# Optimization experiments

Hardware: AMD Instinct MI355X
Metric: run time of the kernel (lower is better)

Reference implementation:

```python
import jax, jax.numpy as jnp
import numpy as np

N = 8192        # num neurons
D = 512         # neuron_state_size
NEG = -1e30     # finite mask value (avoids inf-inf NaNs, matches empty-predecessor -> zero output)


def setup_inputs() -> dict:
    key = jax.random.key(0)
    ks = jax.random.split(key, 5)
    neuron_states = jax.random.normal(ks[0], (N, D), dtype=jnp.float32)
    # sparse-ish directed adjacency; adjacency[i, j] True => i is a predecessor of j
    adjacency = jax.random.bernoulli(ks[1], 0.05, (N, N))
    Wq = jax.random.normal(ks[2], (D, D), dtype=jnp.float32) / np.sqrt(D)
    Wk = jax.random.normal(ks[3], (D, D), dtype=jnp.float32) / np.sqrt(D)
    Wv = jax.random.normal(ks[4], (D, D), dtype=jnp.float32) / np.sqrt(D)
    return {"neuron_states": neuron_states, "adjacency": adjacency, "Wq": Wq, "Wk": Wk, "Wv": Wv}


def reference(neuron_states, adjacency, Wq, Wk, Wv):
    # nn.Linear(bias=False): y = x @ W.T
    q = neuron_states @ Wq.T          # [N, D]
    k = neuron_states @ Wk.T          # [N, D]
    v = neuron_states @ Wv.T          # [N, D]
    # score[j, i] = q_j . k_i, valid iff adjacency[i, j] (i is predecessor of j)
    mask = adjacency.T                # [N_dst, N_src]
    scores = jnp.where(mask, q @ k.T, NEG)
    attn = jax.nn.softmax(scores, axis=1)
    attn = jnp.where(mask, attn, 0.0)  # neurons with no predecessors -> zero output (matches torch empty matmul)
    return attn @ v                   # [N, D]
```

## Files before the change

kernel.cpp:

```cpp
#include <hip/hip_runtime.h>
#include <stdint.h>

#define N 8192
#define D 512
#define NEG -1e30f

typedef _Float16 f16;
typedef f16 f16x4 __attribute__((ext_vector_type(4)));
typedef f16 f16x8 __attribute__((ext_vector_type(8)));
typedef float f32x4v __attribute__((ext_vector_type(4)));
typedef float f32x16 __attribute__((ext_vector_type(16)));

#define XH_OFF   0ull
#define WQH_OFF  (XH_OFF + 8192ull * 512 * 2)
#define WKH_OFF  (WQH_OFF + 512ull * 512 * 2)
#define WVH_OFF  (WKH_OFF + 512ull * 512 * 2)
#define QH_OFF   (WVH_OFF + 512ull * 512 * 2)
#define KH_OFF   (QH_OFF + 8192ull * 512 * 2)
#define VT_OFF   (KH_OFF + 8192ull * 512 * 2)
#define PART_SZ  (8192ull * 512 * 2)
#define P123_OFF (VT_OFF + 8192ull * 512 * 2)

#define QROW     1040
#define QS_OFF   0
#define PROW     144
#define PSB_OFF  66560
#define MLXM_OFF (PSB_OFF + 64 * PROW)
#define MLXL_OFF (MLXM_OFF + 1024)
#define MROW_OFF (MLXL_OFF + 1024)
#define LROW_OFF (MROW_OFF + 256)
#define SCL_OFF  (LROW_OFF + 256)
#define LDSB_V4  (SCL_OFF + 256)

__global__ __launch_bounds__(256) void cvt_fp16(
    const float* __restrict__ X,
    const float* __restrict__ Wq, const float* __restrict__ Wk, const float* __restrict__ Wv,
    f16* __restrict__ Xh,
    f16* __restrict__ Wqh, f16* __restrict__ Wkh, f16* __restrict__ Wvh)
{
    const int idx = blockIdx.x * 256 + threadIdx.x;
    const float* src; f16* dst; int off;
    if (idx < 1048576)      { src = X;  dst = Xh;  off = idx; }
    else if (idx < 1114112) { src = Wq; dst = Wqh; off = idx - 1048576; }
    else if (idx < 1179648) { src = Wk; dst = Wkh; off = idx - 1114112; }
    else                    { src = Wv; dst = Wvh; off = idx - 1179648; }
    const float4 v = ((const float4*)src)[off];
    f16x4 h; h.x = (f16)v.x; h.y = (f16)v.y; h.z = (f16)v.z; h.w = (f16)v.w;
    *(f16x4*)(dst + (size_t)off * 4) = h;
}

__global__ __launch_bounds__(256) void qkv_mfma(
    const f16* __restrict__ Xh,
    const f16* __restrict__ Wqh, const f16* __restrict__ Wkh, const f16* __restrict__ Wvh,
    f16* __restrict__ qh, f16* __restrict__ kh, f16* __restrict__ vt)
{
    const int t    = threadIdx.x;
    const int w    = t >> 6;
    const int lane = t & 63;
    const int lo   = lane & 31;
    const int hi   = lane >> 5;
    const int z    = blockIdx.z;

    int m0, c0; const f16 *Ap, *Bp; f16* Yp; size_t ldy;
    if (z == 2) {
        m0 = blockIdx.x * 128 + w * 32; c0 = blockIdx.y * 128;
        Ap = Wvh; Bp = Xh; Yp = vt; ldy = N;
    } else {
        m0 = blockIdx.y * 128 + w * 32; c0 = blockIdx.x * 128;
        Ap = Xh; Bp = z ? Wkh : Wqh; Yp = z ? kh : qh; ldy = D;
    }

    const f16* arow = Ap + (size_t)(m0 + lo) * D + hi * 8;
    const f16* brow[4];
#pragma unroll
    for (int nn = 0; nn < 4; ++nn)
        brow[nn] = Bp + (size_t)(c0 + nn * 32 + lo) * D + hi * 8;

    f32x16 acc[4];
#pragma unroll
    for (int nn = 0; nn < 4; ++nn)
#pragma unroll
        for (int e = 0; e < 16; ++e) acc[nn][e] = 0.f;

#pragma unroll 4
    for (int ks = 0; ks < 32; ++ks) {
        const f16x8 a = *(const f16x8*)(arow + ks * 16);
#pragma unroll
        for (int nn = 0; nn < 4; ++nn) {
            const f16x8 b = *(const f16x8*)(brow[nn] + ks * 16);
            acc[nn] = __builtin_amdgcn_mfma_f32_32x32x16_f16(a, b, acc[nn], 0, 0, 0);
        }
    }

#pragma unroll
    for (int nn = 0; nn < 4; ++nn)
#pragma unroll
        for (int r = 0; r < 16; ++r) {
            const int row = m0 + (r & 3) + 8 * (r >> 2) + 4 * hi;
            Yp[(size_t)row * ldy + c0 + nn * 32 + lo] = (f16)acc[nn][r];
        }
}

__global__ __launch_bounds__(256, 2) void attn_v4(
    const f16* __restrict__ qh, const f16* __restrict__ kh,
    const f16* __restrict__ vt, const int* __restrict__ adj,
    f16* __restrict__ part0, f16* __restrict__ part123, float2* __restrict__ ml)
{
    extern __shared__ char smem[];
    char*  Qs   = smem + QS_OFF;
    char*  Psb  = smem + PSB_OFF;
    float* mlxm = (float*)(smem + MLXM_OFF);
    float* mlxl = (float*)(smem + MLXL_OFF);
    float* mrow = (float*)(smem + MROW_OFF);
    float* lrow = (float*)(smem + LROW_OFF);
    float* scl  = (float*)(smem + SCL_OFF);

    const int t  = threadIdx.x;
    const int w  = t >> 6;
    const int l  = t & 63;
    const int cl = l & 15;
    const int hq = l >> 4;

    const int nib = gridDim.x >> 7;
    const int b   = blockIdx.x;
    const int xcd = b & 7;
    int ib, jt_;
    if (nib == 4) { ib = xcd >> 1; jt_ = (xcd & 1) * 64 + (b >> 3); }
    else          { ib = xcd >> 2; jt_ = (xcd & 3) * 32 + (b >> 3); }
    const int j0    = jt_ * 64;
    const int ibase = ib * (N / nib);
    const int iters = (N / nib) >> 6;

    f16* pb = (ib == 0) ? part0 : part123 + (size_t)(ib - 1) * ((size_t)N * D);

    for (int c = t; c < 64 * 64; c += 256) {
        const int row = c >> 6, off = c & 63;
        f16x8 v = *(const f16x8*)(qh + (size_t)(j0 + row) * D + off * 8);
        *(f16x8*)(Qs + row * QROW + off * 16) = v;
    }
    if (t < 64) { mrow[t] = NEG; lrow[t] = 0.f; }
    __syncthreads();

    f32x4v oacc[4][8];
#pragma unroll
    for (int jt = 0; jt < 4; ++jt)
#pragma unroll
        for (int dt = 0; dt < 8; ++dt) {
            oacc[jt][dt][0] = 0.f; oacc[jt][dt][1] = 0.f;
            oacc[jt][dt][2] = 0.f; oacc[jt][dt][3] = 0.f;
        }

    const char* qbase[4];
#pragma unroll
    for (int jt = 0; jt < 4; ++jt) qbase[jt] = Qs + (jt * 16 + cl) * QROW;
    const int qoff = hq * 16;

    for (int it = 0; it < iters; ++it) {
        const int i0t = ibase + it * 64;

        f32x4v sacc[4];
#pragma unroll
        for (int jt = 0; jt < 4; ++jt) {
            sacc[jt][0] = 0.f; sacc[jt][1] = 0.f; sacc[jt][2] = 0.f; sacc[jt][3] = 0.f;
        }
        const f16* kp = kh + (size_t)(i0t + w * 16 + cl) * D + hq * 8;
#pragma unroll 4
        for (int ks = 0; ks < 16; ++ks) {
            const f16x8 kf = *(const f16x8*)(kp + ks * 32);
#pragma unroll
            for (int jt = 0; jt < 4; ++jt) {
                const f16x8 qf = *(const f16x8*)(qbase[jt] + ks * 64 + qoff);
                sacc[jt] = __builtin_amdgcn_mfma_f32_16x16x32_f16(kf, qf, sacc[jt], 0, 0, 0);
            }
        }

        const int* ap = adj + (size_t)(i0t + w * 16 + hq * 4) * N + j0 + cl;
        float pe[4][4], mb[4];
#pragma unroll
        for (int jt = 0; jt < 4; ++jt) {
            int mk[4];
#pragma unroll
            for (int r = 0; r < 4; ++r) mk[r] = ap[(size_t)r * N + jt * 16];
            float s[4];
#pragma unroll
            for (int r = 0; r < 4; ++r) s[r] = mk[r] ? sacc[jt][r] : NEG;
            float m4 = fmaxf(fmaxf(s[0], s[1]), fmaxf(s[2], s[3]));
            m4 = fmaxf(m4, __shfl_xor(m4, 16, 64));
            m4 = fmaxf(m4, __shfl_xor(m4, 32, 64));
            mb[jt] = m4;
            float pl = 0.f;
#pragma unroll
            for (int r = 0; r < 4; ++r) {
                const float p = mk[r] ? __expf(s[r] - m4) : 0.f;
                pe[jt][r] = p;
                pl += p;
            }
            pl += __shfl_xor(pl, 16, 64);
            pl += __shfl_xor(pl, 32, 64);
            if (l < 16) {
                mlxm[w * 64 + jt * 16 + l] = m4;
                mlxl[w * 64 + jt * 16 + l] = pl;
            }
        }
        __syncthreads();

        if (t < 64) {
            const float mo = mrow[t];
            const float m0b = mlxm[t],       l0b = mlxl[t];
            const float m1b = mlxm[64 + t],  l1b = mlxl[64 + t];
            const float m2b = mlxm[128 + t], l2b = mlxl[128 + t];
            const float m3b = mlxm[192 + t], l3b = mlxl[192 + t];
            const float mn = fmaxf(mo, fmaxf(fmaxf(m0b, m1b), fmaxf(m2b, m3b)));
            const float ln = lrow[t] * __expf(mo - mn)
                           + l0b * __expf(m0b - mn) + l1b * __expf(m1b - mn)
                           + l2b * __expf(m2b - mn) + l3b * __expf(m3b - mn);
            mrow[t] = mn; lrow[t] = ln; scl[t] = __expf(mo - mn);
        }
        __syncthreads();

#pragma unroll
        for (int jt = 0; jt < 4; ++jt) {
            const f32x4v sc4 = *(const f32x4v*)(scl + jt * 16 + hq * 4);
#pragma unroll
            for (int dt = 0; dt < 8; ++dt) {
                oacc[jt][dt][0] *= sc4[0]; oacc[jt][dt][1] *= sc4[1];
                oacc[jt][dt][2] *= sc4[2]; oacc[jt][dt][3] *= sc4[3];
            }
            const float mn = mrow[jt * 16 + cl];
            const float f  = __expf(mb[jt] - mn);
            union { f16 h[4]; uint2 u; } pc;
#pragma unroll
            for (int r = 0; r < 4; ++r) pc.h[r] = (f16)(pe[jt][r] * f);
            *(uint2*)(Psb + (jt * 16 + cl) * PROW + (w * 16 + hq * 4) * 2) = pc.u;
        }
        __syncthreads();

        f16x8 pa[4][2];
#pragma unroll
        for (int jt = 0; jt < 4; ++jt)
#pragma unroll
            for (int k2 = 0; k2 < 2; ++k2)
                pa[jt][k2] = *(const f16x8*)(Psb + (jt * 16 + cl) * PROW + k2 * 64 + hq * 16);

#pragma unroll
        for (int dt = 0; dt < 8; ++dt) {
            const f16* vp = vt + (size_t)(w * 128 + dt * 16 + cl) * N + i0t + hq * 8;
#pragma unroll
            for (int k2 = 0; k2 < 2; ++k2) {
                const f16x8 vf = *(const f16x8*)(vp + k2 * 32);
#pragma unroll
                for (int jt = 0; jt < 4; ++jt)
                    oacc[jt][dt] = __builtin_amdgcn_mfma_f32_16x16x32_f16(pa[jt][k2], vf, oacc[jt][dt], 0, 0, 0);
            }
        }
        __syncthreads();
    }

#pragma unroll
    for (int jt = 0; jt < 4; ++jt)
#pragma unroll
        for (int dt = 0; dt < 8; ++dt)
#pragma unroll
            for (int r = 0; r < 4; ++r)
                pb[(size_t)(j0 + jt * 16 + hq * 4 + r) * D + w * 128 + dt * 16 + cl] =
                    (f16)oacc[jt][dt][r];
    if (t < 64) {
        float2 v; v.x = mrow[t]; v.y = lrow[t];
        ml[(size_t)ib * N + j0 + t] = v;
    }
}

__global__ __launch_bounds__(256) void merge_p(
    float* __restrict__ out, const f16* __restrict__ p0,
    const f16* __restrict__ p123, const float2* __restrict__ ml, int nib)
{
    const int idx = blockIdx.x * 256 + threadIdx.x;
    const int j = idx >> 7;
    const int col = (idx & 127) * 4;

    float m_g = NEG;
    for (int ib = 0; ib < nib; ++ib) m_g = fmaxf(m_g, ml[(size_t)ib * N + j].x);
    float L = 0.f;
    float4 acc; acc.x = 0.f; acc.y = 0.f; acc.z = 0.f; acc.w = 0.f;
    for (int ib = 0; ib < nib; ++ib) {
        const float2 a = ml[(size_t)ib * N + j];
        const float e = __expf(a.x - m_g);
        L += e * a.y;
        const f16* pp = (ib == 0) ? p0 : p123 + (size_t)(ib - 1) * ((size_t)N * D);
        const f16x4 h = *(const f16x4*)(pp + (size_t)j * D + col);
        acc.x += e * (float)h.x; acc.y += e * (float)h.y;
        acc.z += e * (float)h.z; acc.w += e * (float)h.w;
    }
    const float inv = (L > 0.f) ? 1.f / L : 0.f;
    float4 r; r.x = acc.x * inv; r.y = acc.y * inv; r.z = acc.z * inv; r.w = acc.w * inv;
    ((float4*)out)[idx] = r;
}

extern "C" void kernel_launch(void* const* d_in, const int* in_sizes, int n_in,
                              void* d_out, int out_size, void* d_ws, size_t ws_size,
                              hipStream_t stream) {
    const float* ns  = (const float*)d_in[0];
    const int*   adj = (const int*)d_in[1];
    const float* Wq  = (const float*)d_in[2];
    const float* Wk  = (const float*)d_in[3];
    const float* Wv  = (const float*)d_in[4];

    char* ws = (char*)d_ws;
    f16*   Xh   = (f16*)(ws + XH_OFF);
    f16*   Wqh  = (f16*)(ws + WQH_OFF);
    f16*   Wkh  = (f16*)(ws + WKH_OFF);
    f16*   Wvh  = (f16*)(ws + WVH_OFF);
    f16*   qh   = (f16*)(ws + QH_OFF);
    f16*   kh   = (f16*)(ws + KH_OFF);
    f16*   vt   = (f16*)(ws + VT_OFF);
    f16*   p0   = (f16*)(ws + XH_OFF);
    f16*   p123 = (f16*)(ws + P123_OFF);
    float* out  = (float*)d_out;

    const size_t need4 = P123_OFF + 3 * PART_SZ + 4ull * N * sizeof(float2);
    int nib; size_t ml_off;
    if (ws_size >= need4) { nib = 4; ml_off = P123_OFF + 3 * PART_SZ; }
    else                  { nib = 2; ml_off = P123_OFF + 1 * PART_SZ; }
    float2* mlb = (float2*)(ws + ml_off);

    (void)hipFuncSetAttribute((const void*)attn_v4,
                              hipFuncAttributeMaxDynamicSharedMemorySize, LDSB_V4);

    cvt_fp16<<<4864, 256, 0, stream>>>(ns, Wq, Wk, Wv, Xh, Wqh, Wkh, Wvh);
    qkv_mfma<<<dim3(4, 64, 3), 256, 0, stream>>>(Xh, Wqh, Wkh, Wvh, qh, kh, vt);
    attn_v4<<<128 * nib, 256, LDSB_V4, stream>>>(qh, kh, vt, adj, p0, p123, mlb);
    merge_p<<<4096, 256, 0, stream>>>(out, p0, p123, mlb, nib);
}
```

Measured before the change: 443.7 us.

## Pack adjacency into bitmasks and retile attention to 32 queries x 128 keys

Adds a pre-pass that packs the int32 adjacency matrix into 64-bit ballot masks, so the attention kernel reads one bit per edge instead of a 4-byte int. The attention kernel is retiled to 32 destination rows per block with 128-key steps. Running max and sum now live in registers and are shared via shuffles, which removes one barrier per iteration and the dynamic LDS. Occupancy is raised to 3 blocks per CU. The trade-off is an extra kernel pass over the 256MB adjacency, plus more blocks that each re-read K and V for fewer queries.

```diff
diff --git a/kernel.cpp b/kernel.cpp
--- a/kernel.cpp
+++ b/kernel.cpp
@@ -10,6 +10,7 @@
 typedef f16 f16x8 __attribute__((ext_vector_type(8)));
 typedef float f32x4v __attribute__((ext_vector_type(4)));
 typedef float f32x16 __attribute__((ext_vector_type(16)));
+typedef unsigned long long u64;
 
 #define XH_OFF   0ull
 #define WQH_OFF  (XH_OFF + 8192ull * 512 * 2)
@@ -20,17 +21,11 @@
 #define VT_OFF   (KH_OFF + 8192ull * 512 * 2)
 #define PART_SZ  (8192ull * 512 * 2)
 #define P123_OFF (VT_OFF + 8192ull * 512 * 2)
-
-#define QROW     1040
-#define QS_OFF   0
-#define PROW     144
-#define PSB_OFF  66560
-#define MLXM_OFF (PSB_OFF + 64 * PROW)
-#define MLXL_OFF (MLXM_OFF + 1024)
-#define MROW_OFF (MLXL_OFF + 1024)
-#define LROW_OFF (MROW_OFF + 256)
-#define SCL_OFF  (LROW_OFF + 256)
-#define LDSB_V4  (SCL_OFF + 256)
+#define ML_SZ    (4ull * N * 8)
+#define ADJ_SZ   (128ull * N * 8)
+
+#define QROW 1040
+#define PROW 272
 
 __global__ __launch_bounds__(256) void cvt_fp16(
     const float* __restrict__ X,
@@ -101,19 +96,31 @@
         }
 }
 
-__global__ __launch_bounds__(256, 2) void attn_v4(
+__global__ __launch_bounds__(256) void pack_adj(
+    const int* __restrict__ adj, u64* __restrict__ adjb)
+{
+    const int widx = blockIdx.x;
+    const int wv   = threadIdx.x >> 6;
+    const int lane = threadIdx.x & 63;
+    const int jb   = blockIdx.y * 4096 + wv * 1024;
+    const int* src = adj + (size_t)(widx * 64 + lane) * N;
+    u64* dst = adjb + (size_t)widx * N;
+    for (int jj = 0; jj < 1024; ++jj) {
+        const int j = jb + jj;
+        const u64 m = __ballot(src[j] != 0);
+        if (lane == 0) dst[j] = m;
+    }
+}
+
+__global__ __launch_bounds__(256, 3) void attn_v5(
     const f16* __restrict__ qh, const f16* __restrict__ kh,
-    const f16* __restrict__ vt, const int* __restrict__ adj,
+    const f16* __restrict__ vt, const u64* __restrict__ adjb,
     f16* __restrict__ part0, f16* __restrict__ part123, float2* __restrict__ ml)
 {
-    extern __shared__ char smem[];
-    char*  Qs   = smem + QS_OFF;
-    char*  Psb  = smem + PSB_OFF;
-    float* mlxm = (float*)(smem + MLXM_OFF);
-    float* mlxl = (float*)(smem + MLXL_OFF);
-    float* mrow = (float*)(smem + MROW_OFF);
-    float* lrow = (float*)(smem + LROW_OFF);
-    float* scl  = (float*)(smem + SCL_OFF);
+    __shared__ char  Qs[32 * QROW];
+    __shared__ char  Psb[32 * PROW];
+    __shared__ float mstat[4 * 32];
+    __shared__ float lstat[4 * 32];
 
     const int t  = threadIdx.x;
     const int w  = t >> 6;
@@ -121,135 +128,160 @@
     const int cl = l & 15;
     const int hq = l >> 4;
 
-    const int nib = gridDim.x >> 7;
+    const int nib = gridDim.x >> 8;
     const int b   = blockIdx.x;
     const int xcd = b & 7;
+    const int u   = b >> 3;
     int ib, jt_;
-    if (nib == 4) { ib = xcd >> 1; jt_ = (xcd & 1) * 64 + (b >> 3); }
-    else          { ib = xcd >> 2; jt_ = (xcd & 3) * 32 + (b >> 3); }
-    const int j0    = jt_ * 64;
+    if (nib == 4) { ib = xcd >> 1; jt_ = (xcd & 1) * 128 + u; }
+    else          { ib = xcd >> 2; jt_ = (xcd & 3) * 64 + u; }
+    const int j0    = jt_ * 32;
     const int ibase = ib * (N / nib);
-    const int iters = (N / nib) >> 6;
+    const int iters = (N / nib) >> 7;
 
     f16* pb = (ib == 0) ? part0 : part123 + (size_t)(ib - 1) * ((size_t)N * D);
 
-    for (int c = t; c < 64 * 64; c += 256) {
+    for (int c = t; c < 32 * 64; c += 256) {
         const int row = c >> 6, off = c & 63;
         f16x8 v = *(const f16x8*)(qh + (size_t)(j0 + row) * D + off * 8);
         *(f16x8*)(Qs + row * QROW + off * 16) = v;
     }
-    if (t < 64) { mrow[t] = NEG; lrow[t] = 0.f; }
     __syncthreads();
 
-    f32x4v oacc[4][8];
-#pragma unroll
-    for (int jt = 0; jt < 4; ++jt)
+    float m_run = NEG, l_run = 0.f;
+
+    f32x4v oacc[2][8];
+#pragma unroll
+    for (int jt = 0; jt < 2; ++jt)
 #pragma unroll
         for (int dt = 0; dt < 8; ++dt) {
             oacc[jt][dt][0] = 0.f; oacc[jt][dt][1] = 0.f;
             oacc[jt][dt][2] = 0.f; oacc[jt][dt][3] = 0.f;
         }
 
-    const char* qbase[4];
-#pragma unroll
-    for (int jt = 0; jt < 4; ++jt) qbase[jt] = Qs + (jt * 16 + cl) * QROW;
-    const int qoff = hq * 16;
-
     for (int it = 0; it < iters; ++it) {
-        const int i0t = ibase + it * 64;
-
-        f32x4v sacc[4];
-#pragma unroll
-        for (int jt = 0; jt < 4; ++jt) {
-            sacc[jt][0] = 0.f; sacc[jt][1] = 0.f; sacc[jt][2] = 0.f; sacc[jt][3] = 0.f;
-        }
-        const f16* kp = kh + (size_t)(i0t + w * 16 + cl) * D + hq * 8;
+        const int i0t   = ibase + it * 128;
+        const int iband = i0t + w * 32;
+
+        const u64* ab = adjb + (size_t)(iband >> 6) * N + j0;
+        const u64 wd0 = ab[cl];
+        const u64 wd1 = ab[16 + cl];
+        const int hsh = (w & 1) * 32;
+
+        f32x4v sacc[2][2];
+#pragma unroll
+        for (int a = 0; a < 2; ++a)
+#pragma unroll
+            for (int c2 = 0; c2 < 2; ++c2) {
+                sacc[a][c2][0] = 0.f; sacc[a][c2][1] = 0.f;
+                sacc[a][c2][2] = 0.f; sacc[a][c2][3] = 0.f;
+            }
+        const f16* kp = kh + (size_t)(iband + cl) * D + hq * 8;
 #pragma unroll 4
         for (int ks = 0; ks < 16; ++ks) {
-            const f16x8 kf = *(const f16x8*)(kp + ks * 32);
-#pragma unroll
-            for (int jt = 0; jt < 4; ++jt) {
-                const f16x8 qf = *(const f16x8*)(qbase[jt] + ks * 64 + qoff);
-                sacc[jt] = __builtin_amdgcn_mfma_f32_16x16x32_f16(kf, qf, sacc[jt], 0, 0, 0);
+            const f16x8 kf0 = *(const f16x8*)(kp + ks * 32);
+            const f16x8 kf1 = *(const f16x8*)(kp + (size_t)16 * D + ks * 32);
+            const f16x8 qf0 = *(const f16x8*)(Qs + cl * QROW + ks * 64 + hq * 16);
+            const f16x8 qf1 = *(const f16x8*)(Qs + (16 + cl) * QROW + ks * 64 + hq * 16);
+            sacc[0][0] = __builtin_amdgcn_mfma_f32_16x16x32_f16(kf0, qf0, sacc[0][0], 0, 0, 0);
+            sacc[0][1] = __builtin_amdgcn_mfma_f32_16x16x32_f16(kf0, qf1, sacc[0][1], 0, 0, 0);
+            sacc[1][0] = __builtin_amdgcn_mfma_f32_16x16x32_f16(kf1, qf0, sacc[1][0], 0, 0, 0);
+            sacc[1][1] = __builtin_amdgcn_mfma_f32_16x16x32_f16(kf1, qf1, sacc[1][1], 0, 0, 0);
+        }
+
+        float p[2][2][4];
+        float m4[2], pl[2];
+#pragma unroll
+        for (int jt = 0; jt < 2; ++jt) {
+            const u64 wd = jt ? wd1 : wd0;
+            const uint32_t half_ = (uint32_t)(wd >> hsh);
+            float s[2][4];
+#pragma unroll
+            for (int it2 = 0; it2 < 2; ++it2) {
+                const uint32_t sub = half_ >> (it2 * 16 + hq * 4);
+#pragma unroll
+                for (int r = 0; r < 4; ++r)
+                    s[it2][r] = ((sub >> r) & 1) ? sacc[it2][jt][r] : NEG;
             }
-        }
-
-        const int* ap = adj + (size_t)(i0t + w * 16 + hq * 4) * N + j0 + cl;
-        float pe[4][4], mb[4];
-#pragma unroll
-        for (int jt = 0; jt < 4; ++jt) {
-            int mk[4];
-#pragma unroll
-            for (int r = 0; r < 4; ++r) mk[r] = ap[(size_t)r * N + jt * 16];
-            float s[4];
-#pragma unroll
-            for (int r = 0; r < 4; ++r) s[r] = mk[r] ? sacc[jt][r] : NEG;
-            float m4 = fmaxf(fmaxf(s[0], s[1]), fmaxf(s[2], s[3]));
-            m4 = fmaxf(m4, __shfl_xor(m4, 16, 64));
-            m4 = fmaxf(m4, __shfl_xor(m4, 32, 64));
-            mb[jt] = m4;
-            float pl = 0.f;
-#pragma unroll
-            for (int r = 0; r < 4; ++r) {
-                const float p = mk[r] ? __expf(s[r] - m4) : 0.f;
-                pe[jt][r] = p;
-                pl += p;
+            float m = NEG;
+#pragma unroll
+            for (int it2 = 0; it2 < 2; ++it2)
+#pragma unroll
+                for (int r = 0; r < 4; ++r) m = fmaxf(m, s[it2][r]);
+            m = fmaxf(m, __shfl_xor(m, 16, 64));
+            m = fmaxf(m, __shfl_xor(m, 32, 64));
+            m4[jt] = m;
+            float ps = 0.f;
+#pragma unroll
+            for (int it2 = 0; it2 < 2; ++it2)
+#pragma unroll
+                for (int r = 0; r < 4; ++r) {
+                    const float pe = (s[it2][r] > -1e29f) ? __expf(s[it2][r] - m) : 0.f;
+                    p[it2][jt][r] = pe;
+                    ps += pe;
+                }
+            ps += __shfl_xor(ps, 16, 64);
+            ps += __shfl_xor(ps, 32, 64);
+            pl[jt] = ps;
+        }
+        if (l < 16) {
+            mstat[w * 32 + l]      = m4[0]; lstat[w * 32 + l]      = pl[0];
+            mstat[w * 32 + 16 + l] = m4[1]; lstat[w * 32 + 16 + l] = pl[1];
+        }
+        __syncthreads();
+
+        {
+            const int jj = l & 31;
+            const float b0 = mstat[jj],       s0 = lstat[jj];
+            const float b1 = mstat[32 + jj],  s1 = lstat[32 + jj];
+            const float b2 = mstat[64 + jj],  s2 = lstat[64 + jj];
+            const float b3 = mstat[96 + jj],  s3 = lstat[96 + jj];
+            const float mn = fmaxf(m_run, fmaxf(fmaxf(b0, b1), fmaxf(b2, b3)));
+            const float sc = __expf(m_run - mn);
+            l_run = l_run * sc + s0 * __expf(b0 - mn) + s1 * __expf(b1 - mn)
+                                + s2 * __expf(b2 - mn) + s3 * __expf(b3 - mn);
+            m_run = mn;
+
+#pragma unroll
+            for (int jt = 0; jt < 2; ++jt) {
+                const float mnj = __shfl(mn, jt * 16 + cl, 64);
+                const float f   = __expf(m4[jt] - mnj);
+#pragma unroll
+                for (int it2 = 0; it2 < 2; ++it2) {
+                    union { f16 h[4]; uint2 u2; } pc;
+#pragma unroll
+                    for (int r = 0; r < 4; ++r) pc.h[r] = (f16)(p[it2][jt][r] * f);
+                    *(uint2*)(Psb + (jt * 16 + cl) * PROW +
+                              (w * 32 + it2 * 16 + hq * 4) * 2) = pc.u2;
+                }
             }
-            pl += __shfl_xor(pl, 16, 64);
-            pl += __shfl_xor(pl, 32, 64);
-            if (l < 16) {
-                mlxm[w * 64 + jt * 16 + l] = m4;
-                mlxl[w * 64 + jt * 16 + l] = pl;
-            }
+
+#pragma unroll
+            for (int jt = 0; jt < 2; ++jt)
+#pragma unroll
+                for (int r = 0; r < 4; ++r) {
+                    const float scr = __shfl(sc, jt * 16 + hq * 4 + r, 64);
+#pragma unroll
+                    for (int dt = 0; dt < 8; ++dt) oacc[jt][dt][r] *= scr;
+                }
         }
         __syncthreads();
 
-        if (t < 64) {
-            const float mo = mrow[t];
-            const float m0b = mlxm[t],       l0b = mlxl[t];
-            const float m1b = mlxm[64 + t],  l1b = mlxl[64 + t];
-            const float m2b = mlxm[128 + t], l2b = mlxl[128 + t];
-            const float m3b = mlxm[192 + t], l3b = mlxl[192 + t];
-            const float mn = fmaxf(mo, fmaxf(fmaxf(m0b, m1b), fmaxf(m2b, m3b)));
-            const float ln = lrow[t] * __expf(mo - mn)
-                           + l0b * __expf(m0b - mn) + l1b * __expf(m1b - mn)
-                           + l2b * __expf(m2b - mn) + l3b * __expf(m3b - mn);
-            mrow[t] = mn; lrow[t] = ln; scl[t] = __expf(mo - mn);
-        }
-        __syncthreads();
-
-#pragma unroll
-        for (int jt = 0; jt < 4; ++jt) {
-            const f32x4v sc4 = *(const f32x4v*)(scl + jt * 16 + hq * 4);
-#pragma unroll
-            for (int dt = 0; dt < 8; ++dt) {
-                oacc[jt][dt][0] *= sc4[0]; oacc[jt][dt][1] *= sc4[1];
-                oacc[jt][dt][2] *= sc4[2]; oacc[jt][dt][3] *= sc4[3];
-            }
-            const float mn = mrow[jt * 16 + cl];
-            const float f  = __expf(mb[jt] - mn);
-            union { f16 h[4]; uint2 u; } pc;
-#pragma unroll
-            for (int r = 0; r < 4; ++r) pc.h[r] = (f16)(pe[jt][r] * f);
-            *(uint2*)(Psb + (jt * 16 + cl) * PROW + (w * 16 + hq * 4) * 2) = pc.u;
-        }
-        __syncthreads();
-
-        f16x8 pa[4][2];
-#pragma unroll
-        for (int jt = 0; jt < 4; ++jt)
-#pragma unroll
-            for (int k2 = 0; k2 < 2; ++k2)
+        f16x8 pa[2][4];
+#pragma unroll
+        for (int jt = 0; jt < 2; ++jt)
+#pragma unroll
+            for (int k2 = 0; k2 < 4; ++k2)
                 pa[jt][k2] = *(const f16x8*)(Psb + (jt * 16 + cl) * PROW + k2 * 64 + hq * 16);
 
 #pragma unroll
         for (int dt = 0; dt < 8; ++dt) {
             const f16* vp = vt + (size_t)(w * 128 + dt * 16 + cl) * N + i0t + hq * 8;
 #pragma unroll
-            for (int k2 = 0; k2 < 2; ++k2) {
+            for (int k2 = 0; k2 < 4; ++k2) {
                 const f16x8 vf = *(const f16x8*)(vp + k2 * 32);
 #pragma unroll
-                for (int jt = 0; jt < 4; ++jt)
+                for (int jt = 0; jt < 2; ++jt)
                     oacc[jt][dt] = __builtin_amdgcn_mfma_f32_16x16x32_f16(pa[jt][k2], vf, oacc[jt][dt], 0, 0, 0);
             }
         }
@@ -257,16 +289,16 @@
     }
 
 #pragma unroll
-    for (int jt = 0; jt < 4; ++jt)
+    for (int jt = 0; jt < 2; ++jt)
 #pragma unroll
         for (int dt = 0; dt < 8; ++dt)
 #pragma unroll
             for (int r = 0; r < 4; ++r)
                 pb[(size_t)(j0 + jt * 16 + hq * 4 + r) * D + w * 128 + dt * 16 + cl] =
                     (f16)oacc[jt][dt][r];
-    if (t < 64) {
-        float2 v; v.x = mrow[t]; v.y = lrow[t];
-        ml[(size_t)ib * N + j0 + t] = v;
+    if (w == 0 && l < 32) {
+        float2 v; v.x = m_run; v.y = l_run;
+        ml[(size_t)ib * N + j0 + l] = v;
     }
 }
 
@@ -317,17 +349,16 @@
     f16*   p123 = (f16*)(ws + P123_OFF);
     float* out  = (float*)d_out;
 
-    const size_t need4 = P123_OFF + 3 * PART_SZ + 4ull * N * sizeof(float2);
+    const size_t need4 = P123_OFF + 3 * PART_SZ + ML_SZ + ADJ_SZ;
     int nib; size_t ml_off;
     if (ws_size >= need4) { nib = 4; ml_off = P123_OFF + 3 * PART_SZ; }
     else                  { nib = 2; ml_off = P123_OFF + 1 * PART_SZ; }
-    float2* mlb = (float2*)(ws + ml_off);
-
-    (void)hipFuncSetAttribute((const void*)attn_v4,
-                              hipFuncAttributeMaxDynamicSharedMemorySize, LDSB_V4);
+    float2* mlb  = (float2*)(ws + ml_off);
+    u64*    adjb = (u64*)(ws + ml_off + ML_SZ);
 
     cvt_fp16<<<4864, 256, 0, stream>>>(ns, Wq, Wk, Wv, Xh, Wqh, Wkh, Wvh);
     qkv_mfma<<<dim3(4, 64, 3), 256, 0, stream>>>(Xh, Wqh, Wkh, Wvh, qh, kh, vt);
-    attn_v4<<<128 * nib, 256, LDSB_V4, stream>>>(qh, kh, vt, adj, p0, p123, mlb);
+    pack_adj<<<dim3(128, 2), 256, 0, stream>>>(adj, adjb);
+    attn_v5<<<256 * nib, 256, 0, stream>>>(qh, kh, vt, adjb, p0, p123, mlb);
     merge_p<<<4096, 256, 0, stream>>>(out, p0, p123, mlb, nib);
 }
```

Measured after the change: 892.5 us. 2.01x slower.

## Pack adjacency into bitmasks and prefetch next tile's K and mask

Applied to the files above, without the earlier changes.

Adds a pack_adj kernel that compresses the int32 adjacency matrix into 64-bit ballot masks, so the attention kernel reads one u64 per column per 64-row tile instead of scattered int32 loads. The attention kernel also keeps the running max and sum in registers in every wave, which removes one barrier, skips the output rescale when no scale changed, and prefetches the next tile's mask and half of K during the PV phase. The cost is an extra kernel pass over the 256MB adjacency and more register pressure from the prefetch buffers.

```diff
diff --git a/kernel.cpp b/kernel.cpp
--- a/kernel.cpp
+++ b/kernel.cpp
@@ -10,6 +10,7 @@
 typedef f16 f16x8 __attribute__((ext_vector_type(8)));
 typedef float f32x4v __attribute__((ext_vector_type(4)));
 typedef float f32x16 __attribute__((ext_vector_type(16)));
+typedef unsigned long long u64;
 
 #define XH_OFF   0ull
 #define WQH_OFF  (XH_OFF + 8192ull * 512 * 2)
@@ -20,17 +21,15 @@
 #define VT_OFF   (KH_OFF + 8192ull * 512 * 2)
 #define PART_SZ  (8192ull * 512 * 2)
 #define P123_OFF (VT_OFF + 8192ull * 512 * 2)
+#define ML_SZ    (4ull * N * 8)
+#define ADJ_SZ   (128ull * N * 8)
 
 #define QROW     1040
-#define QS_OFF   0
 #define PROW     144
 #define PSB_OFF  66560
-#define MLXM_OFF (PSB_OFF + 64 * PROW)
-#define MLXL_OFF (MLXM_OFF + 1024)
-#define MROW_OFF (MLXL_OFF + 1024)
-#define LROW_OFF (MROW_OFF + 256)
-#define SCL_OFF  (LROW_OFF + 256)
-#define LDSB_V4  (SCL_OFF + 256)
+#define MST_OFF  75776
+#define LST_OFF  76800
+#define LDSB_V6  77824
 
 __global__ __launch_bounds__(256) void cvt_fp16(
     const float* __restrict__ X,
@@ -101,19 +100,32 @@
         }
 }
 
-__global__ __launch_bounds__(256, 2) void attn_v4(
+__global__ __launch_bounds__(256) void pack_adj(
+    const int* __restrict__ adj, u64* __restrict__ adjb)
+{
+    const int widx = blockIdx.x;
+    const int wv   = threadIdx.x >> 6;
+    const int lane = threadIdx.x & 63;
+    const int jb   = blockIdx.y * 4096 + wv * 1024;
+    const int* src = adj + (size_t)(widx * 64 + lane) * N;
+    u64* dst = adjb + (size_t)widx * N;
+    for (int jj = 0; jj < 1024; ++jj) {
+        const int j = jb + jj;
+        const u64 m = __ballot(src[j] != 0);
+        if (lane == 0) dst[j] = m;
+    }
+}
+
+__global__ __launch_bounds__(256, 2) void attn_v6(
     const f16* __restrict__ qh, const f16* __restrict__ kh,
-    const f16* __restrict__ vt, const int* __restrict__ adj,
+    const f16* __restrict__ vt, const u64* __restrict__ adjb,
     f16* __restrict__ part0, f16* __restrict__ part123, float2* __restrict__ ml)
 {
     extern __shared__ char smem[];
-    char*  Qs   = smem + QS_OFF;
-    char*  Psb  = smem + PSB_OFF;
-    float* mlxm = (float*)(smem + MLXM_OFF);
-    float* mlxl = (float*)(smem + MLXL_OFF);
-    float* mrow = (float*)(smem + MROW_OFF);
-    float* lrow = (float*)(smem + LROW_OFF);
-    float* scl  = (float*)(smem + SCL_OFF);
+    char*  Qs    = smem;
+    char*  Psb   = smem + PSB_OFF;
+    float* mstat = (float*)(smem + MST_OFF);
+    float* lstat = (float*)(smem + LST_OFF);
 
     const int t  = threadIdx.x;
     const int w  = t >> 6;
@@ -138,8 +150,9 @@
         f16x8 v = *(const f16x8*)(qh + (size_t)(j0 + row) * D + off * 8);
         *(f16x8*)(Qs + row * QROW + off * 16) = v;
     }
-    if (t < 64) { mrow[t] = NEG; lrow[t] = 0.f; }
     __syncthreads();
+
+    float m_run = NEG, l_run = 0.f;
 
     f32x4v oacc[4][8];
 #pragma unroll
@@ -150,10 +163,16 @@
             oacc[jt][dt][2] = 0.f; oacc[jt][dt][3] = 0.f;
         }
 
-    const char* qbase[4];
-#pragma unroll
-    for (int jt = 0; jt < 4; ++jt) qbase[jt] = Qs + (jt * 16 + cl) * QROW;
-    const int qoff = hq * 16;
+    u64   wd[4];
+    f16x8 kpre[8];
+    {
+        const u64* ab = adjb + ((size_t)(ibase >> 6)) * N + j0;
+#pragma unroll
+        for (int jt = 0; jt < 4; ++jt) wd[jt] = ab[jt * 16 + cl];
+        const f16* kp = kh + (size_t)(ibase + w * 16 + cl) * D + hq * 8;
+#pragma unroll
+        for (int ks = 0; ks < 8; ++ks) kpre[ks] = *(const f16x8*)(kp + ks * 32);
+    }
 
     for (int it = 0; it < iters; ++it) {
         const int i0t = ibase + it * 64;
@@ -164,76 +183,87 @@
             sacc[jt][0] = 0.f; sacc[jt][1] = 0.f; sacc[jt][2] = 0.f; sacc[jt][3] = 0.f;
         }
         const f16* kp = kh + (size_t)(i0t + w * 16 + cl) * D + hq * 8;
-#pragma unroll 4
+#pragma unroll
         for (int ks = 0; ks < 16; ++ks) {
-            const f16x8 kf = *(const f16x8*)(kp + ks * 32);
+            const f16x8 kf = (ks < 8) ? kpre[ks] : *(const f16x8*)(kp + ks * 32);
 #pragma unroll
             for (int jt = 0; jt < 4; ++jt) {
-                const f16x8 qf = *(const f16x8*)(qbase[jt] + ks * 64 + qoff);
+                const f16x8 qf = *(const f16x8*)(Qs + (jt * 16 + cl) * QROW + ks * 64 + hq * 16);
                 sacc[jt] = __builtin_amdgcn_mfma_f32_16x16x32_f16(kf, qf, sacc[jt], 0, 0, 0);
             }
         }
 
-        const int* ap = adj + (size_t)(i0t + w * 16 + hq * 4) * N + j0 + cl;
-        float pe[4][4], mb[4];
+        float pe[4][4], mb4[4];
 #pragma unroll
         for (int jt = 0; jt < 4; ++jt) {
-            int mk[4];
-#pragma unroll
-            for (int r = 0; r < 4; ++r) mk[r] = ap[(size_t)r * N + jt * 16];
+            const uint32_t sub = (uint32_t)(wd[jt] >> (w * 16 + hq * 4)) & 0xFu;
             float s[4];
 #pragma unroll
-            for (int r = 0; r < 4; ++r) s[r] = mk[r] ? sacc[jt][r] : NEG;
+            for (int r = 0; r < 4; ++r) s[r] = ((sub >> r) & 1) ? sacc[jt][r] : NEG;
             float m4 = fmaxf(fmaxf(s[0], s[1]), fmaxf(s[2], s[3]));
             m4 = fmaxf(m4, __shfl_xor(m4, 16, 64));
             m4 = fmaxf(m4, __shfl_xor(m4, 32, 64));
-            mb[jt] = m4;
+            mb4[jt] = m4;
             float pl = 0.f;
 #pragma unroll
             for (int r = 0; r < 4; ++r) {
-                const float p = mk[r] ? __expf(s[r] - m4) : 0.f;
+                const float p = (s[r] > -1e29f) ? __expf(s[r] - m4) : 0.f;
                 pe[jt][r] = p;
                 pl += p;
             }
             pl += __shfl_xor(pl, 16, 64);
             pl += __shfl_xor(pl, 32, 64);
             if (l < 16) {
-                mlxm[w * 64 + jt * 16 + l] = m4;
-                mlxl[w * 64 + jt * 16 + l] = pl;
+                mstat[w * 64 + jt * 16 + l] = m4;
+                lstat[w * 64 + jt * 16 + l] = pl;
             }
         }
         __syncthreads();
 
-        if (t < 64) {
-            const float mo = mrow[t];
-            const float m0b = mlxm[t],       l0b = mlxl[t];
-            const float m1b = mlxm[64 + t],  l1b = mlxl[64 + t];
-            const float m2b = mlxm[128 + t], l2b = mlxl[128 + t];
-            const float m3b = mlxm[192 + t], l3b = mlxl[192 + t];
-            const float mn = fmaxf(mo, fmaxf(fmaxf(m0b, m1b), fmaxf(m2b, m3b)));
-            const float ln = lrow[t] * __expf(mo - mn)
-                           + l0b * __expf(m0b - mn) + l1b * __expf(m1b - mn)
-                           + l2b * __expf(m2b - mn) + l3b * __expf(m3b - mn);
-            mrow[t] = mn; lrow[t] = ln; scl[t] = __expf(mo - mn);
+        float sc;
+        {
+            const float b0 = mstat[l],       s0 = lstat[l];
+            const float b1 = mstat[64 + l],  s1 = lstat[64 + l];
+            const float b2 = mstat[128 + l], s2 = lstat[128 + l];
+            const float b3 = mstat[192 + l], s3 = lstat[192 + l];
+            const float mn = fmaxf(m_run, fmaxf(fmaxf(b0, b1), fmaxf(b2, b3)));
+            sc = __expf(m_run - mn);
+            l_run = l_run * sc + s0 * __expf(b0 - mn) + s1 * __expf(b1 - mn)
+                               + s2 * __expf(b2 - mn) + s3 * __expf(b3 - mn);
+            m_run = mn;
+        }
+
+#pragma unroll
+        for (int jt = 0; jt < 4; ++jt) {
+            const float mnj = __shfl(m_run, jt * 16 + cl, 64);
+            const float f   = __expf(mb4[jt] - mnj);
+            union { f16 h[4]; uint2 u2; } pc;
+#pragma unroll
+            for (int r = 0; r < 4; ++r) pc.h[r] = (f16)(pe[jt][r] * f);
+            *(uint2*)(Psb + (jt * 16 + cl) * PROW + (w * 16 + hq * 4) * 2) = pc.u2;
+        }
+
+        if (__any(sc != 1.f)) {
+#pragma unroll
+            for (int jt = 0; jt < 4; ++jt)
+#pragma unroll
+                for (int r = 0; r < 4; ++r) {
+                    const float scr = __shfl(sc, jt * 16 + hq * 4 + r, 64);
+#pragma unroll
+                    for (int dt = 0; dt < 8; ++dt) oacc[jt][dt][r] *= scr;
+                }
         }
         __syncthreads();
 
-#pragma unroll
-        for (int jt = 0; jt < 4; ++jt) {
-            const f32x4v sc4 = *(const f32x4v*)(scl + jt * 16 + hq * 4);
-#pragma unroll
-            for (int dt = 0; dt < 8; ++dt) {
-                oacc[jt][dt][0] *= sc4[0]; oacc[jt][dt][1] *= sc4[1];
-                oacc[jt][dt][2] *= sc4[2]; oacc[jt][dt][3] *= sc4[3];
-            }
-            const float mn = mrow[jt * 16 + cl];
-            const float f  = __expf(mb[jt] - mn);
-            union { f16 h[4]; uint2 u; } pc;
-#pragma unroll
-            for (int r = 0; r < 4; ++r) pc.h[r] = (f16)(pe[jt][r] * f);
-            *(uint2*)(Psb + (jt * 16 + cl) * PROW + (w * 16 + hq * 4) * 2) = pc.u;
-        }
-        __syncthreads();
+        if (it + 1 < iters) {
+            const int i0n = i0t + 64;
+            const u64* abn = adjb + ((size_t)(i0n >> 6)) * N + j0;
+#pragma unroll
+            for (int jt = 0; jt < 4; ++jt) wd[jt] = abn[jt * 16 + cl];
+            const f16* kpn = kh + (size_t)(i0n + w * 16 + cl) * D + hq * 8;
+#pragma unroll
+            for (int ks = 0; ks < 8; ++ks) kpre[ks] = *(const f16x8*)(kpn + ks * 32);
+        }
 
         f16x8 pa[4][2];
 #pragma unroll
@@ -265,8 +295,8 @@
                 pb[(size_t)(j0 + jt * 16 + hq * 4 + r) * D + w * 128 + dt * 16 + cl] =
                     (f16)oacc[jt][dt][r];
     if (t < 64) {
-        float2 v; v.x = mrow[t]; v.y = lrow[t];
-        ml[(size_t)ib * N + j0 + t] = v;
+        float2 v; v.x = m_run; v.y = l_run;
+        ml[(size_t)ib * N + j0 + l] = v;
     }
 }
 
@@ -317,17 +347,19 @@
     f16*   p123 = (f16*)(ws + P123_OFF);
     float* out  = (float*)d_out;
 
-    const size_t need4 = P123_OFF + 3 * PART_SZ + 4ull * N * sizeof(float2);
+    const size_t need4 = P123_OFF + 3 * PART_SZ + ML_SZ + ADJ_SZ;
     int nib; size_t ml_off;
     if (ws_size >= need4) { nib = 4; ml_off = P123_OFF + 3 * PART_SZ; }
     else                  { nib = 2; ml_off = P123_OFF + 1 * PART_SZ; }
-    float2* mlb = (float2*)(ws + ml_off);
-
-    (void)hipFuncSetAttribute((const void*)attn_v4,
-                              hipFuncAttributeMaxDynamicSharedMemorySize, LDSB_V4);
+    float2* mlb  = (float2*)(ws + ml_off);
+    u64*    adjb = (u64*)(ws + ml_off + ML_SZ);
+
+    (void)hipFuncSetAttribute((const void*)attn_v6,
+                              hipFuncAttributeMaxDynamicSharedMemorySize, LDSB_V6);
 
     cvt_fp16<<<4864, 256, 0, stream>>>(ns, Wq, Wk, Wv, Xh, Wqh, Wkh, Wvh);
     qkv_mfma<<<dim3(4, 64, 3), 256, 0, stream>>>(Xh, Wqh, Wkh, Wvh, qh, kh, vt);
-    attn_v4<<<128 * nib, 256, LDSB_V4, stream>>>(qh, kh, vt, adj, p0, p123, mlb);
+    pack_adj<<<dim3(128, 2), 256, 0, stream>>>(adj, adjb);
+    attn_v6<<<128 * nib, 256, LDSB_V6, stream>>>(qh, kh, vt, adjb, p0, p123, mlb);
     merge_p<<<4096, 256, 0, stream>>>(out, p0, p123, mlb, nib);
 }
```

Result: slower. 702.5 us (+58.3%).

## Split fused flash attention into materialized scores, row stats, and PV passes

Applied to the files above, without the earlier changes.

Replaces the single online-softmax attention kernel with a multi-pass pipeline. The passes write masked fp16 scores to a workspace buffer, compute per-column max and sum in separate reduction kernels, then run a PV kernel with exact exp and no rescaling or per-iteration syncs. Work is processed in two halves of 4096 destination columns with 8-way source splits. This removes the rescaling and intra-block softmax syncs, but adds a 64MB score matrix round trip through HBM and more kernel launches. fp16 sentinel masking also risks clamping for large scores.

```diff
diff --git a/kernel.cpp b/kernel.cpp
--- a/kernel.cpp
+++ b/kernel.cpp
@@ -4,6 +4,8 @@
 #define N 8192
 #define D 512
 #define NEG -1e30f
+#define JW 4096
+#define SENT -6.0e4f
 
 typedef _Float16 f16;
 typedef f16 f16x4 __attribute__((ext_vector_type(4)));
@@ -18,19 +20,13 @@
 #define QH_OFF   (WVH_OFF + 512ull * 512 * 2)
 #define KH_OFF   (QH_OFF + 8192ull * 512 * 2)
 #define VT_OFF   (KH_OFF + 8192ull * 512 * 2)
-#define PART_SZ  (8192ull * 512 * 2)
-#define P123_OFF (VT_OFF + 8192ull * 512 * 2)
-
-#define QROW     1040
-#define QS_OFF   0
-#define PROW     144
-#define PSB_OFF  66560
-#define MLXM_OFF (PSB_OFF + 64 * PROW)
-#define MLXL_OFF (MLXM_OFF + 1024)
-#define MROW_OFF (MLXL_OFF + 1024)
-#define LROW_OFF (MROW_OFF + 256)
-#define SCL_OFF  (LROW_OFF + 256)
-#define LDSB_V4  (SCL_OFF + 256)
+#define ST_OFF   (VT_OFF + 8192ull * 512 * 2)
+#define MLP_OFF  (ST_OFF + 8192ull * JW * 2)
+#define ML_OFF   (MLP_OFF + 8ull * JW * 8)
+#define PRT_OFF  (ML_OFF + (size_t)JW * 8)
+
+#define QROW 1040
+#define PROW 144
 
 __global__ __launch_bounds__(256) void cvt_fp16(
     const float* __restrict__ X,
@@ -101,19 +97,12 @@
         }
 }
 
-__global__ __launch_bounds__(256, 2) void attn_v4(
+__global__ __launch_bounds__(256, 2) void qk_s(
     const f16* __restrict__ qh, const f16* __restrict__ kh,
-    const f16* __restrict__ vt, const int* __restrict__ adj,
-    f16* __restrict__ part0, f16* __restrict__ part123, float2* __restrict__ ml)
+    const int* __restrict__ adj, f16* __restrict__ St, int jbase)
 {
     extern __shared__ char smem[];
-    char*  Qs   = smem + QS_OFF;
-    char*  Psb  = smem + PSB_OFF;
-    float* mlxm = (float*)(smem + MLXM_OFF);
-    float* mlxl = (float*)(smem + MLXL_OFF);
-    float* mrow = (float*)(smem + MROW_OFF);
-    float* lrow = (float*)(smem + LROW_OFF);
-    float* scl  = (float*)(smem + SCL_OFF);
+    char* Qs = smem;
 
     const int t  = threadIdx.x;
     const int w  = t >> 6;
@@ -121,24 +110,118 @@
     const int cl = l & 15;
     const int hq = l >> 4;
 
-    const int nib = gridDim.x >> 7;
-    const int b   = blockIdx.x;
-    const int xcd = b & 7;
-    int ib, jt_;
-    if (nib == 4) { ib = xcd >> 1; jt_ = (xcd & 1) * 64 + (b >> 3); }
-    else          { ib = xcd >> 2; jt_ = (xcd & 3) * 32 + (b >> 3); }
-    const int j0    = jt_ * 64;
-    const int ibase = ib * (N / nib);
-    const int iters = (N / nib) >> 6;
-
-    f16* pb = (ib == 0) ? part0 : part123 + (size_t)(ib - 1) * ((size_t)N * D);
+    const int j0l  = blockIdx.x * 64;
+    const int jg0  = jbase + j0l;
+    const int ibase = blockIdx.y * 1024;
 
     for (int c = t; c < 64 * 64; c += 256) {
         const int row = c >> 6, off = c & 63;
-        f16x8 v = *(const f16x8*)(qh + (size_t)(j0 + row) * D + off * 8);
+        f16x8 v = *(const f16x8*)(qh + (size_t)(jg0 + row) * D + off * 8);
         *(f16x8*)(Qs + row * QROW + off * 16) = v;
     }
-    if (t < 64) { mrow[t] = NEG; lrow[t] = 0.f; }
+    __syncthreads();
+
+    for (int it = 0; it < 16; ++it) {
+        const int i0t = ibase + it * 64;
+
+        f32x4v sacc[4];
+#pragma unroll
+        for (int jt = 0; jt < 4; ++jt) {
+            sacc[jt][0] = 0.f; sacc[jt][1] = 0.f; sacc[jt][2] = 0.f; sacc[jt][3] = 0.f;
+        }
+        const f16* kp = kh + (size_t)(i0t + w * 16 + cl) * D + hq * 8;
+#pragma unroll
+        for (int ks = 0; ks < 16; ++ks) {
+            const f16x8 kf = *(const f16x8*)(kp + ks * 32);
+#pragma unroll
+            for (int jt = 0; jt < 4; ++jt) {
+                const f16x8 qf = *(const f16x8*)(Qs + (jt * 16 + cl) * QROW + ks * 64 + hq * 16);
+                sacc[jt] = __builtin_amdgcn_mfma_f32_16x16x32_f16(kf, qf, sacc[jt], 0, 0, 0);
+            }
+        }
+
+        const int* ap = adj + (size_t)(i0t + w * 16 + hq * 4) * N + jg0 + cl;
+#pragma unroll
+        for (int jt = 0; jt < 4; ++jt) {
+#pragma unroll
+            for (int r = 0; r < 4; ++r) {
+                const int valid = ap[(size_t)r * N + jt * 16];
+                const float s = valid ? sacc[jt][r] : SENT;
+                St[(size_t)(i0t + w * 16 + hq * 4 + r) * JW + j0l + jt * 16 + cl] = (f16)s;
+            }
+        }
+    }
+}
+
+__global__ __launch_bounds__(256) void rowstat(
+    const f16* __restrict__ St, float2* __restrict__ mlp)
+{
+    __shared__ float mw[4][64];
+    __shared__ float lw[4][64];
+
+    const int t    = threadIdx.x;
+    const int jl   = t & 63;
+    const int isub = t >> 6;
+    const int j0l  = blockIdx.x * 64;
+    const int i0   = blockIdx.y * 1024 + isub * 256;
+
+    float m = NEG, lsum = 0.f;
+    const f16* sp = St + (size_t)i0 * JW + j0l + jl;
+    for (int k = 0; k < 256; ++k) {
+        const float s = (float)sp[(size_t)k * JW];
+        if (s > -5.0e4f) {
+            if (s > m) { lsum = lsum * __expf(m - s) + 1.f; m = s; }
+            else       { lsum += __expf(s - m); }
+        }
+    }
+    mw[isub][jl] = m;
+    lw[isub][jl] = lsum;
+    __syncthreads();
+
+    if (t < 64) {
+        float mg = fmaxf(fmaxf(mw[0][t], mw[1][t]), fmaxf(mw[2][t], mw[3][t]));
+        float lg = lw[0][t] * __expf(mw[0][t] - mg) + lw[1][t] * __expf(mw[1][t] - mg)
+                 + lw[2][t] * __expf(mw[2][t] - mg) + lw[3][t] * __expf(mw[3][t] - mg);
+        float2 v; v.x = mg; v.y = lg;
+        mlp[(size_t)blockIdx.y * JW + j0l + t] = v;
+    }
+}
+
+__global__ __launch_bounds__(256) void combine_ml(
+    const float2* __restrict__ mlp, float2* __restrict__ ml)
+{
+    const int jl = blockIdx.x * 256 + threadIdx.x;
+    float mg = NEG;
+#pragma unroll
+    for (int c = 0; c < 8; ++c) mg = fmaxf(mg, mlp[(size_t)c * JW + jl].x);
+    float lg = 0.f;
+#pragma unroll
+    for (int c = 0; c < 8; ++c) {
+        const float2 a = mlp[(size_t)c * JW + jl];
+        lg += a.y * __expf(a.x - mg);
+    }
+    float2 v; v.x = mg; v.y = lg;
+    ml[jl] = v;
+}
+
+__global__ __launch_bounds__(256, 2) void pv2(
+    const f16* __restrict__ St, const f16* __restrict__ vt,
+    const float2* __restrict__ ml, f16* __restrict__ parts)
+{
+    __shared__ char  Psb[64 * PROW];
+    __shared__ float mloc[64];
+
+    const int t  = threadIdx.x;
+    const int w  = t >> 6;
+    const int l  = t & 63;
+    const int cl = l & 15;
+    const int hq = l >> 4;
+
+    const int j0l   = blockIdx.x * 64;
+    const int ib    = blockIdx.y;
+    const int ibase = ib * 1024;
+
+    if (t < 64) mloc[t] = ml[j0l + t].x;
     __syncthreads();
 
     f32x4v oacc[4][8];
@@ -150,88 +233,28 @@
             oacc[jt][dt][2] = 0.f; oacc[jt][dt][3] = 0.f;
         }
 
-    const char* qbase[4];
-#pragma unroll
-    for (int jt = 0; jt < 4; ++jt) qbase[jt] = Qs + (jt * 16 + cl) * QROW;
-    const int qoff = hq * 16;
-
-    for (int it = 0; it < iters; ++it) {
-        const int i0t = ibase + it * 64;
-
-        f32x4v sacc[4];
-#pragma unroll
-        for (int jt = 0; jt < 4; ++jt) {
-            sacc[jt][0] = 0.f; sacc[jt][1] = 0.f; sacc[jt][2] = 0.f; sacc[jt][3] = 0.f;
-        }
-        const f16* kp = kh + (size_t)(i0t + w * 16 + cl) * D + hq * 8;
-#pragma unroll 4
-        for (int ks = 0; ks < 16; ++ks) {
-            const f16x8 kf = *(const f16x8*)(kp + ks * 32);
-#pragma unroll
-            for (int jt = 0; jt < 4; ++jt) {
-                const f16x8 qf = *(const f16x8*)(qbase[jt] + ks * 64 + qoff);
-                sacc[jt] = __builtin_amdgcn_mfma_f32_16x16x32_f16(kf, qf, sacc[jt], 0, 0, 0);
-            }
-        }
-
-        const int* ap = adj + (size_t)(i0t + w * 16 + hq * 4) * N + j0 + cl;
-        float pe[4][4], mb[4];
-#pragma unroll
-        for (int jt = 0; jt < 4; ++jt) {
-            int mk[4];
-#pragma unroll
-            for (int r = 0; r < 4; ++r) mk[r] = ap[(size_t)r * N + jt * 16];
-            float s[4];
-#pragma unroll
-            for (int r = 0; r < 4; ++r) s[r] = mk[r] ? sacc[jt][r] : NEG;
-            float m4 = fmaxf(fmaxf(s[0], s[1]), fmaxf(s[2], s[3]));
-            m4 = fmaxf(m4, __shfl_xor(m4, 16, 64));
-            m4 = fmaxf(m4, __shfl_xor(m4, 32, 64));
-            mb[jt] = m4;
-            float pl = 0.f;
-#pragma unroll
-            for (int r = 0; r < 4; ++r) {
-                const float p = mk[r] ? __expf(s[r] - m4) : 0.f;
-                pe[jt][r] = p;
-                pl += p;
-            }
-            pl += __shfl_xor(pl, 16, 64);
-            pl += __shfl_xor(pl, 32, 64);
-            if (l < 16) {
-                mlxm[w * 64 + jt * 16 + l] = m4;
-                mlxl[w * 64 + jt * 16 + l] = pl;
-            }
-        }
-        __syncthreads();
-
-        if (t < 64) {
-            const float mo = mrow[t];
-            const float m0b = mlxm[t],       l0b = mlxl[t];
-            const float m1b = mlxm[64 + t],  l1b = mlxl[64 + t];
-            const float m2b = mlxm[128 + t], l2b = mlxl[128 + t];
-            const float m3b = mlxm[192 + t], l3b = mlxl[192 + t];
-            const float mn = fmaxf(mo, fmaxf(fmaxf(m0b, m1b), fmaxf(m2b, m3b)));
-            const float ln = lrow[t] * __expf(mo - mn)
-                           + l0b * __expf(m0b - mn) + l1b * __expf(m1b - mn)
-                           + l2b * __expf(m2b - mn) + l3b * __expf(m3b - mn);
-            mrow[t] = mn; lrow[t] = ln; scl[t] = __expf(mo - mn);
-        }
-        __syncthreads();
-
-#pragma unroll
-        for (int jt = 0; jt < 4; ++jt) {
-            const f32x4v sc4 = *(const f32x4v*)(scl + jt * 16 + hq * 4);
-#pragma unroll
-            for (int dt = 0; dt < 8; ++dt) {
-                oacc[jt][dt][0] *= sc4[0]; oacc[jt][dt][1] *= sc4[1];
-                oacc[jt][dt][2] *= sc4[2]; oacc[jt][dt][3] *= sc4[3];
-            }
-            const float mn = mrow[jt * 16 + cl];
-            const float f  = __expf(mb[jt] - mn);
-            union { f16 h[4]; uint2 u; } pc;
-#pragma unroll
-            for (int r = 0; r < 4; ++r) pc.h[r] = (f16)(pe[jt][r] * f);
-            *(uint2*)(Psb + (jt * 16 + cl) * PROW + (w * 16 + hq * 4) * 2) = pc.u;
+    for (int it = 0; it < 16; ++it) {
+        const int ig0 = ibase + it * 64;
+
+        {
+            const int row = t >> 2, jseg = t & 3;
+            const f16* sp = St + (size_t)(ig0 + row) * JW + j0l + jseg * 16;
+            const f16x8 a = *(const f16x8*)(sp);
+            const f16x8 b = *(const f16x8*)(sp + 8);
+#pragma unroll
+            for (int e = 0; e < 8; ++e) {
+                const int j = jseg * 16 + e;
+                const float s = (float)a[e];
+                const float p = (s > -5.0e4f) ? __expf(s - mloc[j]) : 0.f;
+                *(f16*)(Psb + j * PROW + row * 2) = (f16)p;
+            }
+#pragma unroll
+            for (int e = 0; e < 8; ++e) {
+                const int j = jseg * 16 + 8 + e;
+                const float s = (float)b[e];
+                const float p = (s > -5.0e4f) ? __expf(s - mloc[j]) : 0.f;
+                *(f16*)(Psb + j * PROW + row * 2) = (f16)p;
+            }
         }
         __syncthreads();
 
@@ -244,7 +267,7 @@
 
 #pragma unroll
         for (int dt = 0; dt < 8; ++dt) {
-            const f16* vp = vt + (size_t)(w * 128 + dt * 16 + cl) * N + i0t + hq * 8;
+            const f16* vp = vt + (size_t)(w * 128 + dt * 16 + cl) * N + ig0 + hq * 8;
 #pragma unroll
             for (int k2 = 0; k2 < 2; ++k2) {
                 const f16x8 vf = *(const f16x8*)(vp + k2 * 32);
@@ -256,44 +279,37 @@
         __syncthreads();
     }
 
+    f16* pp = parts + (size_t)ib * ((size_t)JW * D);
 #pragma unroll
     for (int jt = 0; jt < 4; ++jt)
 #pragma unroll
         for (int dt = 0; dt < 8; ++dt)
 #pragma unroll
             for (int r = 0; r < 4; ++r)
-                pb[(size_t)(j0 + jt * 16 + hq * 4 + r) * D + w * 128 + dt * 16 + cl] =
+                pp[(size_t)(j0l + jt * 16 + hq * 4 + r) * D + w * 128 + dt * 16 + cl] =
                     (f16)oacc[jt][dt][r];
-    if (t < 64) {
-        float2 v; v.x = mrow[t]; v.y = lrow[t];
-        ml[(size_t)ib * N + j0 + t] = v;
-    }
-}
-
-__global__ __launch_bounds__(256) void merge_p(
-    float* __restrict__ out, const f16* __restrict__ p0,
-    const f16* __restrict__ p123, const float2* __restrict__ ml, int nib)
+}
+
+__global__ __launch_bounds__(256) void merge_o(
+    float* __restrict__ out, const f16* __restrict__ parts,
+    const float2* __restrict__ ml, int jbase)
 {
     const int idx = blockIdx.x * 256 + threadIdx.x;
-    const int j = idx >> 7;
+    const int jl  = idx >> 7;
     const int col = (idx & 127) * 4;
 
-    float m_g = NEG;
-    for (int ib = 0; ib < nib; ++ib) m_g = fmaxf(m_g, ml[(size_t)ib * N + j].x);
-    float L = 0.f;
     float4 acc; acc.x = 0.f; acc.y = 0.f; acc.z = 0.f; acc.w = 0.f;
-    for (int ib = 0; ib < nib; ++ib) {
-        const float2 a = ml[(size_t)ib * N + j];
-        const float e = __expf(a.x - m_g);
-        L += e * a.y;
-        const f16* pp = (ib == 0) ? p0 : p123 + (size_t)(ib - 1) * ((size_t)N * D);
-        const f16x4 h = *(const f16x4*)(pp + (size_t)j * D + col);
-        acc.x += e * (float)h.x; acc.y += e * (float)h.y;
-        acc.z += e * (float)h.z; acc.w += e * (float)h.w;
-    }
+#pragma unroll
+    for (int ib = 0; ib < 8; ++ib) {
+        const f16x4 h = *(const f16x4*)(parts + (size_t)ib * ((size_t)JW * D)
+                                        + (size_t)jl * D + col);
+        acc.x += (float)h.x; acc.y += (float)h.y;
+        acc.z += (float)h.z; acc.w += (float)h.w;
+    }
+    const float L = ml[jl].y;
     const float inv = (L > 0.f) ? 1.f / L : 0.f;
     float4 r; r.x = acc.x * inv; r.y = acc.y * inv; r.z = acc.z * inv; r.w = acc.w * inv;
-    ((float4*)out)[idx] = r;
+    ((float4*)(out + (size_t)(jbase) * D))[idx] = r;
 }
 
 extern "C" void kernel_launch(void* const* d_in, const int* in_sizes, int n_in,
@@ -306,28 +322,31 @@
     const float* Wv  = (const float*)d_in[4];
 
     char* ws = (char*)d_ws;
-    f16*   Xh   = (f16*)(ws + XH_OFF);
-    f16*   Wqh  = (f16*)(ws + WQH_OFF);
-    f16*   Wkh  = (f16*)(ws + WKH_OFF);
-    f16*   Wvh  = (f16*)(ws + WVH_OFF);
-    f16*   qh   = (f16*)(ws + QH_OFF);
-    f16*   kh   = (f16*)(ws + KH_OFF);
-    f16*   vt   = (f16*)(ws + VT_OFF);
-    f16*   p0   = (f16*)(ws + XH_OFF);
-    f16*   p123 = (f16*)(ws + P123_OFF);
-    float* out  = (float*)d_out;
-
-    const size_t need4 = P123_OFF + 3 * PART_SZ + 4ull * N * sizeof(float2);
-    int nib; size_t ml_off;
-    if (ws_size >= need4) { nib = 4; ml_off = P123_OFF + 3 * PART_SZ; }
-    else                  { nib = 2; ml_off = P123_OFF + 1 * PART_SZ; }
-    float2* mlb = (float2*)(ws + ml_off);
-
-    (void)hipFuncSetAttribute((const void*)attn_v4,
-                              hipFuncAttributeMaxDynamicSharedMemorySize, LDSB_V4);
+    f16*    Xh   = (f16*)(ws + XH_OFF);
+    f16*    Wqh  = (f16*)(ws + WQH_OFF);
+    f16*    Wkh  = (f16*)(ws + WKH_OFF);
+    f16*    Wvh  = (f16*)(ws + WVH_OFF);
+    f16*    qh   = (f16*)(ws + QH_OFF);
+    f16*    kh   = (f16*)(ws + KH_OFF);
+    f16*    vt   = (f16*)(ws + VT_OFF);
+    f16*    St   = (f16*)(ws + ST_OFF);
+    float2* mlp  = (float2*)(ws + MLP_OFF);
+    float2* ml   = (float2*)(ws + ML_OFF);
+    f16*    prt  = (f16*)(ws + PRT_OFF);
+    float*  out  = (float*)d_out;
+
+    (void)hipFuncSetAttribute((const void*)qk_s,
+                              hipFuncAttributeMaxDynamicSharedMemorySize, 64 * QROW);
 
     cvt_fp16<<<4864, 256, 0, stream>>>(ns, Wq, Wk, Wv, Xh, Wqh, Wkh, Wvh);
     qkv_mfma<<<dim3(4, 64, 3), 256, 0, stream>>>(Xh, Wqh, Wkh, Wvh, qh, kh, vt);
-    attn_v4<<<128 * nib, 256, LDSB_V4, stream>>>(qh, kh, vt, adj, p0, p123, mlb);
-    merge_p<<<4096, 256, 0, stream>>>(out, p0, p123, mlb, nib);
-}
+
+    for (int h = 0; h < 2; ++h) {
+        const int jbase = h * JW;
+        qk_s<<<dim3(64, 8), 256, 64 * QROW, stream>>>(qh, kh, adj, St, jbase);
+        rowstat<<<dim3(64, 8), 256, 0, stream>>>(St, mlp);
+        combine_ml<<<16, 256, 0, stream>>>(mlp, ml);
+        pv2<<<dim3(64, 8), 256, 0, stream>>>(St, vt, ml, prt);
+        merge_o<<<2048, 256, 0, stream>>>(out, prt, ml, jbase);
+    }
+}
```

Result: slower. 800.1 us (+80.3%).
